# Performance work log

Hardware: AMD Instinct MI355X
Metric: run time of the kernel (lower is better)

Reference implementation:

```python
import jax, jax.numpy as jnp
import numpy as np

EMB_DIM = 16

def _pos_enc_table(side_len, emb_dim):
    pos = np.arange(side_len)[:, None].astype(np.float64)
    j = np.arange(emb_dim)[None, :]
    enc = pos / np.power(10000.0, 2.0 * (j // 2) / emb_dim)
    enc[0, :] = 0.0
    enc[1:, 0::2] = np.sin(enc[1:, 0::2])
    enc[1:, 1::2] = np.cos(enc[1:, 1::2])
    return enc.astype(np.float32)  # [L, E]

def _pos_embeddings(side_len, emb_dim):
    t = _pos_enc_table(side_len, emb_dim)
    # original uses raw .view (row-major reshape), NOT a transpose
    x = np.tile(t.reshape(1, emb_dim, side_len, 1), (1, 1, 1, side_len))
    y = np.tile(t.reshape(1, emb_dim, 1, side_len), (1, 1, side_len, 1))
    return jnp.asarray(np.concatenate((x, y), axis=1))  # [1, 2E, L, L]

def setup_inputs() -> dict:
    key = jax.random.key(0)
    ks = jax.random.split(key, 7)
    B, C, L = 32, 224, 32
    Cin = C + 2 * EMB_DIM  # 256
    K = V = 256
    s = 0.02
    return {
        "x": jax.random.normal(ks[0], (B, C, L, L), dtype=jnp.float32),
        "wq": jax.random.normal(ks[1], (K, Cin), dtype=jnp.float32) * s,
        "bq": jax.random.normal(ks[2], (K,), dtype=jnp.float32) * s,
        "wk": jax.random.normal(ks[3], (K, Cin), dtype=jnp.float32) * s,
        "bk": jax.random.normal(ks[4], (K,), dtype=jnp.float32) * s,
        "wv": jax.random.normal(ks[5], (V, Cin), dtype=jnp.float32) * s,
        "bv": jax.random.normal(ks[6], (V,), dtype=jnp.float32) * s,
    }

def reference(x, wq, bq, wk, bk, wv, bv):
    B, C, H, W = x.shape
    S = H * W
    Kdim = wq.shape[0]
    Vdim = wv.shape[0]
    pe = _pos_embeddings(H, EMB_DIM).astype(x.dtype)  # [1, 2E, H, W]
    x0 = jnp.concatenate([x, jnp.broadcast_to(pe, (B, 2 * EMB_DIM, H, W))], axis=1)
    x0 = x0.reshape(B, C + 2 * EMB_DIM, S)  # [B, Cin, S]
    # 1x1 conv == channel matmul, then ReLU nonlin
    q = jax.nn.relu(jnp.einsum('kc,bcs->bks', wq, x0) + bq[None, :, None])
    k = jax.nn.relu(jnp.einsum('kc,bcs->bks', wk, x0) + bk[None, :, None])
    v = jax.nn.relu(jnp.einsum('vc,bcs->bvs', wv, x0) + bv[None, :, None])
    attn = jnp.einsum('bks,bkt->bst', q, k) / jnp.sqrt(jnp.asarray(Kdim, x.dtype))
    mask = jnp.tril(jnp.ones((S, S), dtype=x.dtype))  # causal incl. self
    attn = attn * mask + (1.0 - mask) * (-10000.0)
    attn = jax.nn.softmax(attn, axis=-1) * mask  # double masking as in source
    out1 = jnp.einsum('bst,bvt->bvs', attn, v)  # [B, V, S]
    # NOTE: source computes out1 + fc(out1) but then overwrites with out1.view(...)
    return out1.reshape(B, Vdim, H, W)
```

## Files before the change

### kernel.cpp

```cpp
#include <hip/hip_runtime.h>
#include <cstdint>

typedef float  f32x4  __attribute__((ext_vector_type(4)));
typedef short  short8 __attribute__((ext_vector_type(8)));
typedef _Float16 half4 __attribute__((ext_vector_type(4)));
typedef _Float16 half8 __attribute__((ext_vector_type(8)));

__device__ __forceinline__ unsigned short f2bf(float f) {
    unsigned u = __builtin_bit_cast(unsigned, f);
    u += 0x7FFFu + ((u >> 16) & 1u);
    return (unsigned short)(u >> 16);
}

__global__ void wconv_kernel(const float* __restrict__ wq,
                             const float* __restrict__ wk,
                             const float* __restrict__ wv,
                             unsigned short* __restrict__ Wb) {
    int p = blockIdx.x >> 8;
    int i = ((blockIdx.x & 255) << 8) + threadIdx.x;
    const float* src = (p == 0) ? wq : ((p == 1) ? wk : wv);
    Wb[(p << 16) + i] = f2bf(src[i]);
}

__global__ __launch_bounds__(256, 2) void fproj_kernel(
        const float* __restrict__ x,
        const unsigned short* __restrict__ Wb,
        const float* __restrict__ bq, const float* __restrict__ bk,
        const float* __restrict__ bv,
        unsigned short* __restrict__ Q, unsigned short* __restrict__ K,
        _Float16* __restrict__ V) {
    __shared__ __align__(16) char Xlds[32768];
    __shared__ __align__(16) char Wlds[32768];
    float* Tt = (float*)Wlds;

    int st = blockIdx.x;
    int b  = blockIdx.y;
    int sb = st << 6;
    int tid = threadIdx.x; int w = tid >> 6; int l = tid & 63;
    int g = l >> 4, c = l & 15;
    int wr = w >> 1, wc = w & 1;

    #pragma unroll 1
    for (int sc = 0; sc < 2; ++sc) {
        if (sc) __syncthreads();
        #pragma unroll
        for (int r = 0; r < 28; ++r) {
            int idx = r * 256 + tid;
            int cc = idx >> 5, lo = idx & 31;
            Tt[cc * 33 + lo] = x[((b * 224 + cc) << 10) + sb + (sc << 5) + lo];
        }
        __syncthreads();
        #pragma unroll
        for (int r = 0; r < 4; ++r) {
            int idx = r * 256 + tid;
            if (idx < 896) {
                int cc16 = idx >> 5;
                int sl = idx & 31;
                int s = (sc << 5) + sl;
                short8 v8;
                #pragma unroll
                for (int j = 0; j < 8; ++j)
                    v8[j] = (short)f2bf(Tt[(cc16 * 8 + j) * 33 + sl]);
                *(short8*)&Xlds[(s << 9) + ((cc16 ^ (s & 7)) << 4)] = v8;
            }
        }
        if (tid < 128) {
            int sl = tid >> 2;
            int cc16 = 28 + (tid & 3);
            int s = (sc << 5) + sl;
            int sg = sb + s;
            int h = sg >> 5, ww = sg & 31;
            short8 v8;
            #pragma unroll
            for (int j = 0; j < 8; ++j) {
                int ch = (cc16 - 28) * 8 + j;
                int i = (ch < 16) ? (ch * 32 + h) : ((ch - 16) * 32 + ww);
                int ll = i >> 4, e = i & 15;
                float val = 0.f;
                if (ll > 0) {
                    float ang = (float)ll * powf(10000.f, -(float)(e >> 1) * 0.125f);
                    val = (e & 1) ? cosf(ang) : sinf(ang);
                }
                v8[j] = (short)f2bf(val);
            }
            *(short8*)&Xlds[(s << 9) + ((cc16 ^ (s & 7)) << 4)] = v8;
        }
    }
    __syncthreads();

    short8 af[2][8];
    #pragma unroll
    for (int i = 0; i < 2; ++i) {
        const char* ab = &Xlds[(wr * 32 + i * 16 + c) << 9];
        #pragma unroll
        for (int kk = 0; kk < 8; ++kk)
            af[i][kk] = *(const short8*)&ab[((kk * 4 + g) ^ (c & 7)) << 4];
    }

    #pragma unroll 1
    for (int pj = 0; pj < 3; ++pj) {
        const float* bias = (pj == 0) ? bq : ((pj == 1) ? bk : bv);
        #pragma unroll 1
        for (int ot = 0; ot < 4; ++ot) {
            const unsigned short* Wg = Wb + (pj << 16) + (ot << 14);
            #pragma unroll
            for (int p = 0; p < 8; ++p) {
                int ch = p * 256 + tid;
                int row = ch >> 5;
                int cl = (ch & 31) ^ (row & 7);
                __builtin_amdgcn_global_load_lds(
                    (const unsigned int*)&Wg[(row << 8) + cl * 8],
                    (unsigned int*)(Wlds + ((p << 8) + (w << 6)) * 16), 16, 0, 0);
            }
            asm volatile("s_waitcnt vmcnt(0)\n\ts_barrier" ::: "memory");

            f32x4 acc[2][2];
            #pragma unroll
            for (int i = 0; i < 2; ++i)
                #pragma unroll
                for (int j = 0; j < 2; ++j) acc[i][j] = (f32x4){0.f, 0.f, 0.f, 0.f};

            const char* bb0 = &Wlds[(wc * 32 + c) << 9];
            const char* bb1 = &Wlds[(wc * 32 + 16 + c) << 9];
            __builtin_amdgcn_s_setprio(1);
            #pragma unroll
            for (int kk = 0; kk < 8; ++kk) {
                int co = ((kk * 4 + g) ^ (c & 7)) << 4;
                short8 b0 = *(const short8*)&bb0[co];
                short8 b1 = *(const short8*)&bb1[co];
                acc[0][0] = __builtin_amdgcn_mfma_f32_16x16x32_bf16(af[0][kk], b0, acc[0][0], 0, 0, 0);
                acc[0][1] = __builtin_amdgcn_mfma_f32_16x16x32_bf16(af[0][kk], b1, acc[0][1], 0, 0, 0);
                acc[1][0] = __builtin_amdgcn_mfma_f32_16x16x32_bf16(af[1][kk], b0, acc[1][0], 0, 0, 0);
                acc[1][1] = __builtin_amdgcn_mfma_f32_16x16x32_bf16(af[1][kk], b1, acc[1][1], 0, 0, 0);
            }
            __builtin_amdgcn_s_setprio(0);

            #pragma unroll
            for (int j = 0; j < 2; ++j) {
                int o = (ot << 6) + wc * 32 + j * 16 + c;
                float bbv = bias[o];
                #pragma unroll
                for (int i = 0; i < 2; ++i) {
                    int sgb = sb + wr * 32 + i * 16;
                    if (pj < 2) {
                        unsigned short* dst = (pj == 0) ? Q : K;
                        #pragma unroll
                        for (int r = 0; r < 4; ++r) {
                            float v = fmaxf(acc[i][j][r] + bbv, 0.f);
                            int s = sgb + 4 * g + r;
                            dst[(((b << 10) + s) << 8) + o] = f2bf(v);
                        }
                    } else {
                        half4 hv;
                        #pragma unroll
                        for (int r = 0; r < 4; ++r)
                            hv[r] = (_Float16)fmaxf(acc[i][j][r] + bbv, 0.f);
                        int hi = (sgb >> 4) & 1;
                        int tt = sgb >> 5;
                        *(half4*)&V[((size_t)((b << 5) + tt) << 13)
                                    + ((o << 2) + (g ^ ((o >> 1) & 3))) * 8
                                    + (hi << 2)] = hv;
                    }
                }
            }
            __syncthreads();
        }
    }
}

__global__ __launch_bounds__(256, 2) void attn_kernel(
        const unsigned short* __restrict__ Q,
        const unsigned short* __restrict__ K,
        const _Float16* __restrict__ V,
        float* __restrict__ out) {
    __shared__ __align__(16) char Klds[2][16384];
    __shared__ __align__(16) char Vlds[2][16384];

    int bid = blockIdx.x;
    int xcd  = bid & 7;
    int qv   = (bid >> 3) & 7;
    int bhi  = (bid >> 6) & 3;
    int hf   = bid >> 8;
    int b  = (bhi << 3) | xcd;
    int qt = hf ? qv : (15 - qv);

    int tid = threadIdx.x; int w = tid >> 6; int l = tid & 63;
    int g = l >> 4, c = l & 15;
    int s0 = (qt << 6) + (w << 4);

    short8 qf[8];
    #pragma unroll
    for (int kk = 0; kk < 8; ++kk)
        qf[kk] = *(const short8*)&Q[(((b << 10) + s0 + c) << 8) + kk * 32 + g * 8];

    float m = -1e30f, lsum = 0.f;
    f32x4 acc[16];
    #pragma unroll
    for (int i = 0; i < 16; ++i) acc[i] = (f32x4){0.f, 0.f, 0.f, 0.f};

    const unsigned short* Kb_ = &K[(size_t)b << 18];
    const _Float16*       Vb_ = &V[(size_t)b << 18];

    int nt = 2 * qt + 2;
    int dt = 2 * qt + (w >> 1);

    auto stage = [&](int t, int bufi) {
        int t0 = t << 5;
        #pragma unroll
        for (int j = 0; j < 4; ++j) {
            int ch = (j << 8) + tid;
            int trow = ch >> 5;
            int cl = (ch & 31) ^ (trow & 7);
            __builtin_amdgcn_global_load_lds(
                (const unsigned int*)&Kb_[((t0 + trow) << 8) + cl * 8],
                (unsigned int*)(Klds[bufi] + ((j << 8) + (w << 6)) * 16), 16, 0, 0);
        }
        #pragma unroll
        for (int j = 0; j < 4; ++j) {
            int ch = (j << 8) + tid;
            __builtin_amdgcn_global_load_lds(
                (const unsigned int*)&Vb_[((size_t)t << 13) + ch * 8],
                (unsigned int*)(Vlds[bufi] + ((j << 8) + (w << 6)) * 16), 16, 0, 0);
        }
    };

    stage(0, 0);

    for (int t = 0; t < nt; ++t) {
        asm volatile("s_waitcnt vmcnt(0)\n\ts_barrier" ::: "memory");
        if (t + 1 < nt) stage(t + 1, (t + 1) & 1);
        if (t > dt) continue;

        const char* Kl = Klds[t & 1];
        const char* Vl = Vlds[t & 1];
        half8 vread[16];
        #pragma unroll
        for (int vt = 0; vt < 16; ++vt) {
            int pos = (vt << 6) + (c << 2) + (g ^ ((c >> 1) & 3));
            vread[vt] = *(const half8*)&Vl[pos << 4];
        }
        #pragma unroll
        for (int sub = 0; sub < 2; ++sub) {
            bool dmask = (t == dt) && (sub == (w & 1));
            if ((t == dt) && !(w & 1) && sub == 1) break;
            int toff = sub << 4;
            f32x4 sc0 = {0.f,0.f,0.f,0.f}, sc1 = {0.f,0.f,0.f,0.f};
            const char* kbase = &Kl[(toff + c) * 512];
            __builtin_amdgcn_s_setprio(1);
            #pragma unroll
            for (int kk = 0; kk < 8; kk += 2) {
                short8 a0 = *(const short8*)&kbase[(((kk * 4 + g)       ^ (c & 7)) << 4)];
                short8 a1 = *(const short8*)&kbase[((((kk + 1) * 4 + g) ^ (c & 7)) << 4)];
                sc0 = __builtin_amdgcn_mfma_f32_16x16x32_bf16(a0, qf[kk], sc0, 0, 0, 0);
                sc1 = __builtin_amdgcn_mfma_f32_16x16x32_bf16(a1, qf[kk + 1], sc1, 0, 0, 0);
            }
            __builtin_amdgcn_s_setprio(0);
            float sv[4];
            #pragma unroll
            for (int r = 0; r < 4; ++r) sv[r] = (sc0[r] + sc1[r]) * 0.0625f;
            if (dmask) {
                #pragma unroll
                for (int r = 0; r < 4; ++r)
                    if (4 * g + r > c) sv[r] = -1e30f;
            }
            float tm = fmaxf(fmaxf(sv[0], sv[1]), fmaxf(sv[2], sv[3]));
            if (!__all((int)(tm <= m + 8.f))) {
                float tr = fmaxf(tm, __shfl_xor(tm, 16));
                tr = fmaxf(tr, __shfl_xor(tr, 32));
                float mnew = fmaxf(m, tr);
                float alpha = __expf(m - mnew);
                m = mnew;
                lsum *= alpha;
                #pragma unroll
                for (int i = 0; i < 16; ++i) acc[i] *= alpha;
            }
            float p[4];
            #pragma unroll
            for (int r = 0; r < 4; ++r) { p[r] = __expf(sv[r] - m); lsum += p[r]; }
            half4 pb;
            #pragma unroll
            for (int r = 0; r < 4; ++r) pb[r] = (_Float16)p[r];
            __builtin_amdgcn_s_setprio(1);
            #pragma unroll
            for (int vt = 0; vt < 16; ++vt) {
                half4 vf;
                #pragma unroll
                for (int jj = 0; jj < 4; ++jj) vf[jj] = vread[vt][sub * 4 + jj];
                acc[vt] = __builtin_amdgcn_mfma_f32_16x16x16f16(vf, pb, acc[vt], 0, 0, 0);
            }
            __builtin_amdgcn_s_setprio(0);
        }
    }

    lsum += __shfl_xor(lsum, 16);
    lsum += __shfl_xor(lsum, 32);
    float rl = 1.f / lsum;
    #pragma unroll
    for (int vt = 0; vt < 16; ++vt) {
        #pragma unroll
        for (int r = 0; r < 4; ++r)
            out[(((b << 8) + vt * 16 + 4 * g + r) << 10) + s0 + c] = acc[vt][r] * rl;
    }
}

extern "C" void kernel_launch(void* const* d_in, const int* in_sizes, int n_in,
                              void* d_out, int out_size, void* d_ws, size_t ws_size,
                              hipStream_t stream) {
    const float* x  = (const float*)d_in[0];
    const float* wq = (const float*)d_in[1];
    const float* bq = (const float*)d_in[2];
    const float* wk = (const float*)d_in[3];
    const float* bk = (const float*)d_in[4];
    const float* wv = (const float*)d_in[5];
    const float* bv = (const float*)d_in[6];
    float* out = (float*)d_out;

    char* ws = (char*)d_ws;
    unsigned short* Wb = (unsigned short*)ws;
    unsigned short* Qb = (unsigned short*)(ws + 393216);
    unsigned short* Kb = (unsigned short*)(ws + 393216 + 16777216);
    _Float16*       Vb = (_Float16*)     (ws + 393216 + 2 * 16777216);

    wconv_kernel<<<768, 256, 0, stream>>>(wq, wk, wv, Wb);
    fproj_kernel<<<dim3(16, 32), 256, 0, stream>>>(x, Wb, bq, bk, bv, Qb, Kb, Vb);
    attn_kernel<<<512, 256, 0, stream>>>(Qb, Kb, Vb, out);
}
```

Baseline: 99.65 us.

## Pre-swizzle weights into MFMA fragment layout and read B operands directly from global

```diff
diff --git a/kernel.cpp b/kernel.cpp
--- a/kernel.cpp
+++ b/kernel.cpp
@@ -15,23 +15,31 @@
 __global__ void wconv_kernel(const float* __restrict__ wq,
                              const float* __restrict__ wk,
                              const float* __restrict__ wv,
-                             unsigned short* __restrict__ Wb) {
-    int p = blockIdx.x >> 8;
-    int i = ((blockIdx.x & 255) << 8) + threadIdx.x;
-    const float* src = (p == 0) ? wq : ((p == 1) ? wk : wv);
-    Wb[(p << 16) + i] = f2bf(src[i]);
+                             unsigned short* __restrict__ Wf) {
+    int t = (blockIdx.x << 8) + threadIdx.x;
+    int l = t & 63;
+    int frag = t >> 6;
+    int kk = frag & 7;
+    int o16 = (frag >> 3) & 15;
+    int pj = frag >> 7;
+    int c = l & 15, g = l >> 4;
+    const float* src = (pj == 0) ? wq : ((pj == 1) ? wk : wv);
+    const float* s = &src[(o16 * 16 + c) * 256 + kk * 32 + g * 8];
+    short8 v;
+    #pragma unroll
+    for (int j = 0; j < 8; ++j) v[j] = (short)f2bf(s[j]);
+    *(short8*)&Wf[(size_t)t * 8] = v;
 }
 
 __global__ __launch_bounds__(256, 2) void fproj_kernel(
         const float* __restrict__ x,
-        const unsigned short* __restrict__ Wb,
+        const unsigned short* __restrict__ Wf,
         const float* __restrict__ bq, const float* __restrict__ bk,
         const float* __restrict__ bv,
         unsigned short* __restrict__ Q, unsigned short* __restrict__ K,
         _Float16* __restrict__ V) {
     __shared__ __align__(16) char Xlds[32768];
-    __shared__ __align__(16) char Wlds[32768];
-    float* Tt = (float*)Wlds;
+    __shared__ __align__(16) float Tt[224 * 33];
 
     int st = blockIdx.x;
     int b  = blockIdx.y;
@@ -102,32 +110,21 @@
         const float* bias = (pj == 0) ? bq : ((pj == 1) ? bk : bv);
         #pragma unroll 1
         for (int ot = 0; ot < 4; ++ot) {
-            const unsigned short* Wg = Wb + (pj << 16) + (ot << 14);
-            #pragma unroll
-            for (int p = 0; p < 8; ++p) {
-                int ch = p * 256 + tid;
-                int row = ch >> 5;
-                int cl = (ch & 31) ^ (row & 7);
-                __builtin_amdgcn_global_load_lds(
-                    (const unsigned int*)&Wg[(row << 8) + cl * 8],
-                    (unsigned int*)(Wlds + ((p << 8) + (w << 6)) * 16), 16, 0, 0);
-            }
-            asm volatile("s_waitcnt vmcnt(0)\n\ts_barrier" ::: "memory");
-
             f32x4 acc[2][2];
             #pragma unroll
             for (int i = 0; i < 2; ++i)
                 #pragma unroll
                 for (int j = 0; j < 2; ++j) acc[i][j] = (f32x4){0.f, 0.f, 0.f, 0.f};
 
-            const char* bb0 = &Wlds[(wc * 32 + c) << 9];
-            const char* bb1 = &Wlds[(wc * 32 + 16 + c) << 9];
+            const short8* B0 = (const short8*)&Wf[
+                (size_t)((pj * 16 + ot * 4 + wc * 2 + 0) * 8) * 512 + l * 8];
+            const short8* B1 = (const short8*)&Wf[
+                (size_t)((pj * 16 + ot * 4 + wc * 2 + 1) * 8) * 512 + l * 8];
             __builtin_amdgcn_s_setprio(1);
             #pragma unroll
             for (int kk = 0; kk < 8; ++kk) {
-                int co = ((kk * 4 + g) ^ (c & 7)) << 4;
-                short8 b0 = *(const short8*)&bb0[co];
-                short8 b1 = *(const short8*)&bb1[co];
+                short8 b0 = B0[kk * 64];
+                short8 b1 = B1[kk * 64];
                 acc[0][0] = __builtin_amdgcn_mfma_f32_16x16x32_bf16(af[0][kk], b0, acc[0][0], 0, 0, 0);
                 acc[0][1] = __builtin_amdgcn_mfma_f32_16x16x32_bf16(af[0][kk], b1, acc[0][1], 0, 0, 0);
                 acc[1][0] = __builtin_amdgcn_mfma_f32_16x16x32_bf16(af[1][kk], b0, acc[1][0], 0, 0, 0);
@@ -163,7 +160,6 @@
                     }
                 }
             }
-            __syncthreads();
         }
     }
 }
@@ -316,12 +312,12 @@
     float* out = (float*)d_out;
 
     char* ws = (char*)d_ws;
-    unsigned short* Wb = (unsigned short*)ws;
+    unsigned short* Wf = (unsigned short*)ws;
     unsigned short* Qb = (unsigned short*)(ws + 393216);
     unsigned short* Kb = (unsigned short*)(ws + 393216 + 16777216);
     _Float16*       Vb = (_Float16*)     (ws + 393216 + 2 * 16777216);
 
-    wconv_kernel<<<768, 256, 0, stream>>>(wq, wk, wv, Wb);
-    fproj_kernel<<<dim3(16, 32), 256, 0, stream>>>(x, Wb, bq, bk, bv, Qb, Kb, Vb);
+    wconv_kernel<<<96, 256, 0, stream>>>(wq, wk, wv, Wf);
+    fproj_kernel<<<dim3(16, 32), 256, 0, stream>>>(x, Wf, bq, bk, bv, Qb, Kb, Vb);
     attn_kernel<<<512, 256, 0, stream>>>(Qb, Kb, Vb, out);
 }
```

New measurement: 105.9 us. 1.06x slower.

## Double-buffer weight tiles in projection kernel, reusing the input LDS buffer

Applied to the files above, without the earlier changes.

```diff
diff --git a/kernel.cpp b/kernel.cpp
--- a/kernel.cpp
+++ b/kernel.cpp
@@ -96,74 +96,80 @@
         for (int kk = 0; kk < 8; ++kk)
             af[i][kk] = *(const short8*)&ab[((kk * 4 + g) ^ (c & 7)) << 4];
     }
+    __syncthreads();
+
+    auto stageW = [&](int i, char* dstb) {
+        const unsigned short* Wg = Wb + ((i >> 2) << 16) + ((i & 3) << 14);
+        #pragma unroll
+        for (int p = 0; p < 8; ++p) {
+            int ch = p * 256 + tid;
+            int row = ch >> 5;
+            int cl = (ch & 31) ^ (row & 7);
+            __builtin_amdgcn_global_load_lds(
+                (const unsigned int*)&Wg[(row << 8) + cl * 8],
+                (unsigned int*)(dstb + ((p << 8) + (w << 6)) * 16), 16, 0, 0);
+        }
+    };
+
+    stageW(0, Xlds);
 
     #pragma unroll 1
-    for (int pj = 0; pj < 3; ++pj) {
+    for (int i = 0; i < 12; ++i) {
+        asm volatile("s_waitcnt vmcnt(0)\n\ts_barrier" ::: "memory");
+        if (i + 1 < 12) stageW(i + 1, ((i + 1) & 1) ? Wlds : Xlds);
+        const char* Wl = (i & 1) ? Wlds : Xlds;
+        int pj = i >> 2;
+        int ot = i & 3;
         const float* bias = (pj == 0) ? bq : ((pj == 1) ? bk : bv);
-        #pragma unroll 1
-        for (int ot = 0; ot < 4; ++ot) {
-            const unsigned short* Wg = Wb + (pj << 16) + (ot << 14);
-            #pragma unroll
-            for (int p = 0; p < 8; ++p) {
-                int ch = p * 256 + tid;
-                int row = ch >> 5;
-                int cl = (ch & 31) ^ (row & 7);
-                __builtin_amdgcn_global_load_lds(
-                    (const unsigned int*)&Wg[(row << 8) + cl * 8],
-                    (unsigned int*)(Wlds + ((p << 8) + (w << 6)) * 16), 16, 0, 0);
-            }
-            asm volatile("s_waitcnt vmcnt(0)\n\ts_barrier" ::: "memory");
-
-            f32x4 acc[2][2];
-            #pragma unroll
-            for (int i = 0; i < 2; ++i)
-                #pragma unroll
-                for (int j = 0; j < 2; ++j) acc[i][j] = (f32x4){0.f, 0.f, 0.f, 0.f};
-
-            const char* bb0 = &Wlds[(wc * 32 + c) << 9];
-            const char* bb1 = &Wlds[(wc * 32 + 16 + c) << 9];
-            __builtin_amdgcn_s_setprio(1);
-            #pragma unroll
-            for (int kk = 0; kk < 8; ++kk) {
-                int co = ((kk * 4 + g) ^ (c & 7)) << 4;
-                short8 b0 = *(const short8*)&bb0[co];
-                short8 b1 = *(const short8*)&bb1[co];
-                acc[0][0] = __builtin_amdgcn_mfma_f32_16x16x32_bf16(af[0][kk], b0, acc[0][0], 0, 0, 0);
-                acc[0][1] = __builtin_amdgcn_mfma_f32_16x16x32_bf16(af[0][kk], b1, acc[0][1], 0, 0, 0);
-                acc[1][0] = __builtin_amdgcn_mfma_f32_16x16x32_bf16(af[1][kk], b0, acc[1][0], 0, 0, 0);
-                acc[1][1] = __builtin_amdgcn_mfma_f32_16x16x32_bf16(af[1][kk], b1, acc[1][1], 0, 0, 0);
-            }
-            __builtin_amdgcn_s_setprio(0);
-
-            #pragma unroll
-            for (int j = 0; j < 2; ++j) {
-                int o = (ot << 6) + wc * 32 + j * 16 + c;
-                float bbv = bias[o];
-                #pragma unroll
-                for (int i = 0; i < 2; ++i) {
-                    int sgb = sb + wr * 32 + i * 16;
-                    if (pj < 2) {
-                        unsigned short* dst = (pj == 0) ? Q : K;
-                        #pragma unroll
-                        for (int r = 0; r < 4; ++r) {
-                            float v = fmaxf(acc[i][j][r] + bbv, 0.f);
-                            int s = sgb + 4 * g + r;
-                            dst[(((b << 10) + s) << 8) + o] = f2bf(v);
-                        }
-                    } else {
-                        half4 hv;
-                        #pragma unroll
-                        for (int r = 0; r < 4; ++r)
-                            hv[r] = (_Float16)fmaxf(acc[i][j][r] + bbv, 0.f);
-                        int hi = (sgb >> 4) & 1;
-                        int tt = sgb >> 5;
-                        *(half4*)&V[((size_t)((b << 5) + tt) << 13)
-                                    + ((o << 2) + (g ^ ((o >> 1) & 3))) * 8
-                                    + (hi << 2)] = hv;
+
+        f32x4 acc[2][2];
+        #pragma unroll
+        for (int i1 = 0; i1 < 2; ++i1)
+            #pragma unroll
+            for (int j = 0; j < 2; ++j) acc[i1][j] = (f32x4){0.f, 0.f, 0.f, 0.f};
+
+        const char* bb0 = &Wl[(wc * 32 + c) << 9];
+        const char* bb1 = &Wl[(wc * 32 + 16 + c) << 9];
+        __builtin_amdgcn_s_setprio(1);
+        #pragma unroll
+        for (int kk = 0; kk < 8; ++kk) {
+            int co = ((kk * 4 + g) ^ (c & 7)) << 4;
+            short8 b0 = *(const short8*)&bb0[co];
+            short8 b1 = *(const short8*)&bb1[co];
+            acc[0][0] = __builtin_amdgcn_mfma_f32_16x16x32_bf16(af[0][kk], b0, acc[0][0], 0, 0, 0);
+            acc[0][1] = __builtin_amdgcn_mfma_f32_16x16x32_bf16(af[0][kk], b1, acc[0][1], 0, 0, 0);
+            acc[1][0] = __builtin_amdgcn_mfma_f32_16x16x32_bf16(af[1][kk], b0, acc[1][0], 0, 0, 0);
+            acc[1][1] = __builtin_amdgcn_mfma_f32_16x16x32_bf16(af[1][kk], b1, acc[1][1], 0, 0, 0);
+        }
+        __builtin_amdgcn_s_setprio(0);
+
+        #pragma unroll
+        for (int j = 0; j < 2; ++j) {
+            int o = (ot << 6) + wc * 32 + j * 16 + c;
+            float bbv = bias[o];
+            #pragma unroll
+            for (int i2 = 0; i2 < 2; ++i2) {
+                int sgb = sb + wr * 32 + i2 * 16;
+                if (pj < 2) {
+                    unsigned short* dst = (pj == 0) ? Q : K;
+                    #pragma unroll
+                    for (int r = 0; r < 4; ++r) {
+                        float v = fmaxf(acc[i2][j][r] + bbv, 0.f);
+                        int s = sgb + 4 * g + r;
+                        dst[(((b << 10) + s) << 8) + o] = f2bf(v);
                     }
+                } else {
+                    half4 hv;
+                    #pragma unroll
+                    for (int r = 0; r < 4; ++r)
+                        hv[r] = (_Float16)fmaxf(acc[i2][j][r] + bbv, 0.f);
+                    int hi = (sgb >> 4) & 1;
+                    int tt = sgb >> 5;
+                    *(half4*)&V[((size_t)((b << 5) + tt) << 13)
+                                + ((o << 2) + (g ^ ((o >> 1) & 3))) * 8
+                                + (hi << 2)] = hv;
                 }
             }
-            __syncthreads();
         }
     }
 }
```

Measured after the change: 100.2 us. About the same (+0.6%).

## Split attention K tiles to 16 rows with deeper K prefetch pipeline

Applied to the files above, without the earlier changes.

```diff
diff --git a/kernel.cpp b/kernel.cpp
--- a/kernel.cpp
+++ b/kernel.cpp
@@ -173,7 +173,7 @@
         const unsigned short* __restrict__ K,
         const _Float16* __restrict__ V,
         float* __restrict__ out) {
-    __shared__ __align__(16) char Klds[2][16384];
+    __shared__ __align__(16) char Klds[4][8192];
     __shared__ __align__(16) char Vlds[2][16384];
 
     int bid = blockIdx.x;
@@ -201,13 +201,14 @@
     const unsigned short* Kb_ = &K[(size_t)b << 18];
     const _Float16*       Vb_ = &V[(size_t)b << 18];
 
-    int nt = 2 * qt + 2;
-    int dt = 2 * qt + (w >> 1);
-
-    auto stage = [&](int t, int bufi) {
-        int t0 = t << 5;
-        #pragma unroll
-        for (int j = 0; j < 4; ++j) {
+    int nt = 4 * qt + 4;
+    int dt = 4 * qt + w;
+    int mlast = 2 * qt + 1;
+
+    auto stageK = [&](int t16, int bufi) {
+        int t0 = t16 << 4;
+        #pragma unroll
+        for (int j = 0; j < 2; ++j) {
             int ch = (j << 8) + tid;
             int trow = ch >> 5;
             int cl = (ch & 31) ^ (trow & 7);
@@ -215,81 +216,94 @@
                 (const unsigned int*)&Kb_[((t0 + trow) << 8) + cl * 8],
                 (unsigned int*)(Klds[bufi] + ((j << 8) + (w << 6)) * 16), 16, 0, 0);
         }
+    };
+    auto stageV = [&](int m32, int bufi) {
         #pragma unroll
         for (int j = 0; j < 4; ++j) {
             int ch = (j << 8) + tid;
             __builtin_amdgcn_global_load_lds(
-                (const unsigned int*)&Vb_[((size_t)t << 13) + ch * 8],
+                (const unsigned int*)&Vb_[((size_t)m32 << 13) + ch * 8],
                 (unsigned int*)(Vlds[bufi] + ((j << 8) + (w << 6)) * 16), 16, 0, 0);
         }
     };
 
-    stage(0, 0);
+    stageK(0, 0);
+    stageV(0, 0);
+    stageK(1, 1);
+
+    half4 vlo[16], vhi[16];
 
     for (int t = 0; t < nt; ++t) {
-        asm volatile("s_waitcnt vmcnt(0)\n\ts_barrier" ::: "memory");
-        if (t + 1 < nt) stage(t + 1, (t + 1) & 1);
+        if (t & 1) asm volatile("s_waitcnt vmcnt(6)\n\ts_barrier" ::: "memory");
+        else       asm volatile("s_waitcnt vmcnt(2)\n\ts_barrier" ::: "memory");
+        int tk = (t + 2 < nt) ? (t + 2) : (nt - 1);
+        stageK(tk, (t + 2) & 3);
+        if (!(t & 1)) {
+            int mm = t >> 1;
+            int m1r = mm + 1;
+            bool real = (m1r <= mlast);
+            stageV(real ? m1r : mm, real ? (m1r & 1) : ((mm & 1) ^ 1));
+        }
         if (t > dt) continue;
 
-        const char* Kl = Klds[t & 1];
-        const char* Vl = Vlds[t & 1];
-        half8 vread[16];
-        #pragma unroll
-        for (int vt = 0; vt < 16; ++vt) {
-            int pos = (vt << 6) + (c << 2) + (g ^ ((c >> 1) & 3));
-            vread[vt] = *(const half8*)&Vl[pos << 4];
-        }
-        #pragma unroll
-        for (int sub = 0; sub < 2; ++sub) {
-            bool dmask = (t == dt) && (sub == (w & 1));
-            if ((t == dt) && !(w & 1) && sub == 1) break;
-            int toff = sub << 4;
-            f32x4 sc0 = {0.f,0.f,0.f,0.f}, sc1 = {0.f,0.f,0.f,0.f};
-            const char* kbase = &Kl[(toff + c) * 512];
-            __builtin_amdgcn_s_setprio(1);
-            #pragma unroll
-            for (int kk = 0; kk < 8; kk += 2) {
-                short8 a0 = *(const short8*)&kbase[(((kk * 4 + g)       ^ (c & 7)) << 4)];
-                short8 a1 = *(const short8*)&kbase[((((kk + 1) * 4 + g) ^ (c & 7)) << 4)];
-                sc0 = __builtin_amdgcn_mfma_f32_16x16x32_bf16(a0, qf[kk], sc0, 0, 0, 0);
-                sc1 = __builtin_amdgcn_mfma_f32_16x16x32_bf16(a1, qf[kk + 1], sc1, 0, 0, 0);
-            }
-            __builtin_amdgcn_s_setprio(0);
-            float sv[4];
-            #pragma unroll
-            for (int r = 0; r < 4; ++r) sv[r] = (sc0[r] + sc1[r]) * 0.0625f;
-            if (dmask) {
-                #pragma unroll
-                for (int r = 0; r < 4; ++r)
-                    if (4 * g + r > c) sv[r] = -1e30f;
-            }
-            float tm = fmaxf(fmaxf(sv[0], sv[1]), fmaxf(sv[2], sv[3]));
-            if (!__all((int)(tm <= m + 8.f))) {
-                float tr = fmaxf(tm, __shfl_xor(tm, 16));
-                tr = fmaxf(tr, __shfl_xor(tr, 32));
-                float mnew = fmaxf(m, tr);
-                float alpha = __expf(m - mnew);
-                m = mnew;
-                lsum *= alpha;
-                #pragma unroll
-                for (int i = 0; i < 16; ++i) acc[i] *= alpha;
-            }
-            float p[4];
-            #pragma unroll
-            for (int r = 0; r < 4; ++r) { p[r] = __expf(sv[r] - m); lsum += p[r]; }
-            half4 pb;
-            #pragma unroll
-            for (int r = 0; r < 4; ++r) pb[r] = (_Float16)p[r];
-            __builtin_amdgcn_s_setprio(1);
+        const char* Kl = Klds[t & 3];
+        if (!(t & 1)) {
+            const char* Vl = Vlds[(t >> 1) & 1];
             #pragma unroll
             for (int vt = 0; vt < 16; ++vt) {
-                half4 vf;
-                #pragma unroll
-                for (int jj = 0; jj < 4; ++jj) vf[jj] = vread[vt][sub * 4 + jj];
-                acc[vt] = __builtin_amdgcn_mfma_f32_16x16x16f16(vf, pb, acc[vt], 0, 0, 0);
-            }
-            __builtin_amdgcn_s_setprio(0);
-        }
+                int pos = (vt << 6) + (c << 2) + (g ^ ((c >> 1) & 3));
+                half8 vr = *(const half8*)&Vl[pos << 4];
+                vlo[vt] = (half4){vr[0], vr[1], vr[2], vr[3]};
+                vhi[vt] = (half4){vr[4], vr[5], vr[6], vr[7]};
+            }
+        }
+        f32x4 sc0 = {0.f,0.f,0.f,0.f}, sc1 = {0.f,0.f,0.f,0.f};
+        const char* kbase = &Kl[c * 512];
+        __builtin_amdgcn_s_setprio(1);
+        #pragma unroll
+        for (int kk = 0; kk < 8; kk += 2) {
+            short8 a0 = *(const short8*)&kbase[(((kk * 4 + g)       ^ (c & 7)) << 4)];
+            short8 a1 = *(const short8*)&kbase[((((kk + 1) * 4 + g) ^ (c & 7)) << 4)];
+            sc0 = __builtin_amdgcn_mfma_f32_16x16x32_bf16(a0, qf[kk], sc0, 0, 0, 0);
+            sc1 = __builtin_amdgcn_mfma_f32_16x16x32_bf16(a1, qf[kk + 1], sc1, 0, 0, 0);
+        }
+        __builtin_amdgcn_s_setprio(0);
+        float sv[4];
+        #pragma unroll
+        for (int r = 0; r < 4; ++r) sv[r] = (sc0[r] + sc1[r]) * 0.0625f;
+        if (t == dt) {
+            #pragma unroll
+            for (int r = 0; r < 4; ++r)
+                if (4 * g + r > c) sv[r] = -1e30f;
+        }
+        float tm = fmaxf(fmaxf(sv[0], sv[1]), fmaxf(sv[2], sv[3]));
+        if (!__all((int)(tm <= m + 8.f))) {
+            float tr = fmaxf(tm, __shfl_xor(tm, 16));
+            tr = fmaxf(tr, __shfl_xor(tr, 32));
+            float mnew = fmaxf(m, tr);
+            float alpha = __expf(m - mnew);
+            m = mnew;
+            lsum *= alpha;
+            #pragma unroll
+            for (int i = 0; i < 16; ++i) acc[i] *= alpha;
+        }
+        float p[4];
+        #pragma unroll
+        for (int r = 0; r < 4; ++r) { p[r] = __expf(sv[r] - m); lsum += p[r]; }
+        half4 pb;
+        #pragma unroll
+        for (int r = 0; r < 4; ++r) pb[r] = (_Float16)p[r];
+        __builtin_amdgcn_s_setprio(1);
+        if (t & 1) {
+            #pragma unroll
+            for (int vt = 0; vt < 16; ++vt)
+                acc[vt] = __builtin_amdgcn_mfma_f32_16x16x16f16(vhi[vt], pb, acc[vt], 0, 0, 0);
+        } else {
+            #pragma unroll
+            for (int vt = 0; vt < 16; ++vt)
+                acc[vt] = __builtin_amdgcn_mfma_f32_16x16x16f16(vlo[vt], pb, acc[vt], 0, 0, 0);
+        }
+        __builtin_amdgcn_s_setprio(0);
     }
 
     lsum += __shfl_xor(lsum, 16);
```

After: 117.3 us. 17.7% more time.
